# Performance work log

Hardware: AMD Instinct MI355X
Metric: run time of the kernel (lower is better)

## Reference

```python
import jax, jax.numpy as jnp
import numpy as np

S, G, N, E = 4, 3, 20000, 320000   # seq_len, num_graphs, nodes, edges
DIN = HID = OUT = 64


def setup_inputs() -> dict:
    key = jax.random.key(0)
    ks = jax.random.split(key, 12)
    s = 0.1  # weight scale ~ Glorot-ish for d=64
    return {
        "x": jax.random.normal(ks[0], (S, G, N, DIN), jnp.float32),
        "edge_index": jax.random.randint(ks[1], (S, G, 2, E), 0, N, dtype=jnp.int32),
        "W1l": jax.random.normal(ks[2], (G, DIN, HID), jnp.float32) * s,
        "W1r": jax.random.normal(ks[3], (G, DIN, HID), jnp.float32) * s,
        "b1": jnp.zeros((G, HID), jnp.float32),
        "W2l": jax.random.normal(ks[4], (G, HID, OUT), jnp.float32) * s,
        "W2r": jax.random.normal(ks[5], (G, HID, OUT), jnp.float32) * s,
        "b2": jnp.zeros((G, OUT), jnp.float32),
        "Wih": jax.random.normal(ks[6], (4 * OUT, OUT), jnp.float32) * s,
        "Whh": jax.random.normal(ks[7], (4 * OUT, OUT), jnp.float32) * s,
        "bih": jnp.zeros((4 * OUT,), jnp.float32),
        "bhh": jnp.zeros((4 * OUT,), jnp.float32),
    }


def _sage(x, ei, Wl, Wr, b):
    # PyG SAGEConv(aggr='mean'): out = mean_{j->i}(x_j) @ Wl + x_i @ Wr + b
    src, dst = ei[0], ei[1]
    n = x.shape[0]
    msg = jax.ops.segment_sum(x[src], dst, num_segments=n)          # [N, d]
    cnt = jax.ops.segment_sum(jnp.ones((ei.shape[1], 1), x.dtype), dst, num_segments=n)
    mean = jnp.where(cnt > 0, msg / jnp.maximum(cnt, 1.0), 0.0)
    return mean @ Wl + x @ Wr + b


def _gnn(x, ei, Wl1, Wr1, bb1, Wl2, Wr2, bb2):
    h = jnp.tanh(_sage(x, ei, Wl1, Wr1, bb1))
    return jnp.tanh(_sage(h, ei, Wl2, Wr2, bb2))


def reference(x, edge_index, W1l, W1r, b1, W2l, W2r, b2, Wih, Whh, bih, bhh):
    # vmap over graphs (each graph has its own conv weights), then over timesteps
    per_graph = jax.vmap(_gnn, in_axes=(0, 0, 0, 0, 0, 0, 0, 0))
    per_seq = jax.vmap(per_graph, in_axes=(0, 0, None, None, None, None, None, None))
    h = per_seq(x, edge_index, W1l, W1r, b1, W2l, W2r, b2)          # [S, G, N, OUT]
    # torch: per timestep stack graphs [G,N,O] -> transpose -> [N,G,O]; cat over seq on dim0
    lstm_in = jnp.transpose(h, (0, 2, 1, 3)).reshape(S * N, G, OUT)  # [B, T=G, OUT]
    B = lstm_in.shape[0]

    def step(carry, xt):
        hp, cp = carry
        gates = xt @ Wih.T + hp @ Whh.T + bih + bhh                 # [B, 4*OUT]
        i, f, g, o = jnp.split(gates, 4, axis=-1)                   # torch gate order i,f,g,o
        c = jax.nn.sigmoid(f) * cp + jax.nn.sigmoid(i) * jnp.tanh(g)
        hn = jax.nn.sigmoid(o) * jnp.tanh(c)
        return (hn, c), None

    init = (jnp.zeros((B, OUT), x.dtype), jnp.zeros((B, OUT), x.dtype))
    (h_last, _), _ = jax.lax.scan(step, init, jnp.transpose(lstm_in, (1, 0, 2)))
    return h_last  # [S*N, OUT] == lstm_out[:, -1, :].squeeze()
```

## Files before the change

kernel.cpp:

```cpp
#include <hip/hip_runtime.h>
#include <math.h>

#define S 4
#define G 3
#define NN 20000
#define EE 320000
#define D 64
#define SG (S*G)

#define RGS 32
#define RNODES2 625
#define BCAP 12000
#define CHUNKA 100

#define LTILES 314
#define LTASKS (12*LTILES)
#define LPERX  (LTASKS/8)

static __device__ __forceinline__ float rcpf(float x){ return __builtin_amdgcn_rcpf(x); }
static __device__ __forceinline__ float sigmf(float x){ return rcpf(1.0f + __expf(-x)); }
static __device__ __forceinline__ float tanhf_fast(float x){
    float t = __expf(2.0f*x);
    return 1.0f - 2.0f*rcpf(t + 1.0f);
}

static __device__ __forceinline__ unsigned short f2bf(float f){
    union { float f; unsigned u; } v; v.f = f;
    unsigned r = v.u + 0x7FFF + ((v.u >> 16) & 1);
    return (unsigned short)(r >> 16);
}

typedef short bf16x8 __attribute__((ext_vector_type(8)));
typedef float f32x4  __attribute__((ext_vector_type(4)));


__global__ __launch_bounds__(256) void binA_kernel(const int* __restrict__ ei,
                                                   int* __restrict__ bcur,
                                                   int* __restrict__ bkt){
    __shared__ int wcnt[4*RGS];
    __shared__ int wb[4*RGS];
    int chunk = blockIdx.x, sg = blockIdx.y;
    int tid = threadIdx.x, w = tid >> 6;
    const int* srcp = ei + (size_t)(sg*2 + 0)*EE;
    const int* dstp = ei + (size_t)(sg*2 + 1)*EE;
    const int EPC = EE/CHUNKA;
    int start = chunk*EPC, end = start + EPC;

    for (int it = 0; it < (EPC + 1023)/1024; ++it){
        if (tid < 4*RGS) wcnt[tid] = 0;
        __syncthreads();
        int e = start + it*1024 + tid*4;
        bool valid = e < end;
        int d_[4], s_[4], r_[4], dl_[4], rk_[4];
        if (valid){
            int4 d4 = *(const int4*)&dstp[e];
            int4 s4 = *(const int4*)&srcp[e];
            d_[0]=d4.x; d_[1]=d4.y; d_[2]=d4.z; d_[3]=d4.w;
            s_[0]=s4.x; s_[1]=s4.y; s_[2]=s4.z; s_[3]=s4.w;
            #pragma unroll
            for (int j = 0; j < 4; ++j){
                int r = d_[j] / RNODES2;
                r_[j]  = r;
                dl_[j] = d_[j] - r*RNODES2;
                rk_[j] = atomicAdd(&wcnt[w*RGS + r], 1);
            }
        }
        __syncthreads();
        if (tid < RGS){
            int c0 = wcnt[0*RGS+tid], c1 = wcnt[1*RGS+tid];
            int c2 = wcnt[2*RGS+tid], c3 = wcnt[3*RGS+tid];
            int tot = c0+c1+c2+c3;
            int gb = 0;
            if (tot > 0) gb = atomicAdd(&bcur[sg*RGS + tid], tot);
            wb[0*RGS+tid] = gb;
            wb[1*RGS+tid] = gb + c0;
            wb[2*RGS+tid] = gb + c0 + c1;
            wb[3*RGS+tid] = gb + c0 + c1 + c2;
        }
        __syncthreads();
        if (valid){
            #pragma unroll
            for (int j = 0; j < 4; ++j){
                int pos = wb[w*RGS + r_[j]] + rk_[j];
                if (pos < BCAP)
                    bkt[(size_t)(sg*RGS + r_[j])*BCAP + pos] = (dl_[j] << 15) | s_[j];
            }
        }
    }
}


__global__ __launch_bounds__(256) void buildB_kernel(int* __restrict__ bkt,
                                                     const int* __restrict__ bcur,
                                                     int* __restrict__ off2,
                                                     int* __restrict__ deg2){
    __shared__ int hist[RNODES2];
    __shared__ int pref[RNODES2];
    __shared__ int seg[BCAP];
    __shared__ int sums[256];
    int sg = blockIdx.x / RGS, rg = blockIdx.x % RGS;
    int tid = threadIdx.x;
    int cnt = bcur[sg*RGS + rg];
    if (cnt > BCAP) cnt = BCAP;
    size_t base = (size_t)(sg*RGS + rg)*BCAP;

    for (int i = tid; i < RNODES2; i += 256) hist[i] = 0;
    __syncthreads();
    for (int j = tid; j < cnt; j += 256)
        atomicAdd(&hist[bkt[base + j] >> 15], 1);
    __syncthreads();

    int lo = tid*3, hi = min(lo+3, RNODES2);
    int s = 0;
    for (int i = lo; i < hi; ++i) s += hist[i];
    sums[tid] = s; __syncthreads();
    for (int ofs = 1; ofs < 256; ofs <<= 1){
        int v = (tid >= ofs) ? sums[tid-ofs] : 0;
        __syncthreads();
        sums[tid] += v;
        __syncthreads();
    }
    int run = sums[tid] - s;
    int gnode = sg*NN + rg*RNODES2;
    for (int i = lo; i < hi; ++i){
        pref[i] = run;
        off2[gnode + i] = (int)base + run;
        deg2[gnode + i] = hist[i];
        run += hist[i];
    }
    __syncthreads();

    for (int j = tid; j < cnt; j += 256){
        int p = bkt[base + j];
        int slot = atomicAdd(&pref[p >> 15], 1);
        seg[slot] = p & 0x7FFF;
    }
    __syncthreads();

    for (int j = tid; j < cnt; j += 256) bkt[base + j] = seg[j];
}


__global__ __launch_bounds__(256) void convert_kernel(const float* __restrict__ x,
                                                      unsigned short* __restrict__ xb){
    int idx = blockIdx.x*256 + threadIdx.x;
    if (idx >= SG*NN*16) return;
    float4 v = ((const float4*)x)[idx];
    uint2 pk;
    pk.x = (unsigned)f2bf(v.x) | ((unsigned)f2bf(v.y) << 16);
    pk.y = (unsigned)f2bf(v.z) | ((unsigned)f2bf(v.w) << 16);
    ((uint2*)xb)[idx] = pk;
}


__global__ __launch_bounds__(256) void wprep2_kernel(const float* __restrict__ W1l,
                                                     const float* __restrict__ W1r,
                                                     const float* __restrict__ W2l,
                                                     const float* __restrict__ W2r,
                                                     const float* __restrict__ Wih,
                                                     const float* __restrict__ Whh,
                                                     const float* __restrict__ bih,
                                                     const float* __restrict__ bhh,
                                                     unsigned short* __restrict__ WL1,
                                                     unsigned short* __restrict__ WL2,
                                                     unsigned short* __restrict__ Wt,
                                                     float* __restrict__ bc){
    int idx = blockIdx.x*256 + threadIdx.x;
    if (idx < 24576){
        int g = idx >> 13, rem = idx & 8191, col = rem >> 7, k = rem & 127;
        float v = (k < 64) ? W1l[((size_t)g*64 + k)*64 + col]
                           : W1r[((size_t)g*64 + (k-64))*64 + col];
        WL1[idx] = f2bf(v);
    } else if (idx < 49152){
        int t = idx - 24576;
        int g = t >> 13, rem = t & 8191, col = rem >> 7, k = rem & 127;
        float v = (k < 64) ? W2l[((size_t)g*64 + k)*64 + col]
                           : W2r[((size_t)g*64 + (k-64))*64 + col];
        WL2[t] = f2bf(v);
    } else if (idx < 81920){
        int t = idx - 49152;
        int col = t >> 7, k = t & 127;
        float v = (k < 64) ? Wih[col*64 + k] : Whh[col*64 + (k - 64)];
        Wt[t] = f2bf(v);
    } else if (idx < 82176){
        int t = idx - 81920;
        bc[t] = bih[t] + bhh[t];
    }
}


#define WP 72

__global__ __launch_bounds__(256) void layer_kernel(const unsigned short* __restrict__ xb,
                                                    const int* __restrict__ off2,
                                                    const int* __restrict__ deg2,
                                                    const int* __restrict__ csr,
                                                    const unsigned short* __restrict__ WL,
                                                    const float* __restrict__ bias,
                                                    unsigned short* __restrict__ outb){
    __shared__ unsigned short sM[4][16*WP];
    __shared__ unsigned short sO[4][16*WP];
    int L = blockIdx.x;
    int xcd = L & 7, k = L >> 3;
    int task = xcd*LPERX + k;
    int sg = task / LTILES;
    int tile = task - sg*LTILES;
    if (tile >= (NN + 63)/64) return;
    int g = sg % G;
    int tid = threadIdx.x;
    int row0 = tile*64;
    const unsigned short* inb = xb + (size_t)sg*NN*D;

    int wave = tid >> 6, lane = tid & 63;
    int i0 = row0 + wave*16;

    {
        int gp = lane >> 3, fl = lane & 7;
        int ii = min(i0 + (lane & 15), NN-1);
        int val = (lane < 16) ? off2[sg*NN + ii] : ((lane < 32) ? deg2[sg*NN + ii] : 0);
        int r0loc = gp, r1loc = 8 + gp;
        int a0  = __shfl(val, r0loc, 64);
        int dg0 = __shfl(val, 16 + r0loc, 64);
        int a1  = __shfl(val, r1loc, 64);
        int dg1 = __shfl(val, 16 + r1loc, 64);
        if (i0 + r0loc >= NN) dg0 = 0;
        if (i0 + r1loc >= NN) dg1 = 0;
        float acc0[8] = {0,0,0,0,0,0,0,0};
        float acc1[8] = {0,0,0,0,0,0,0,0};
        int mx = max(dg0, dg1);
        for (int base = 0; base < mx; base += 8){
            int my0 = 0, my1 = 0;
            if (base + fl < dg0) my0 = csr[a0 + base + fl];
            if (base + fl < dg1) my1 = csr[a1 + base + fl];
            uint4 v0[8], v1[8];
            #pragma unroll
            for (int j = 0; j < 8; ++j){
                int n0j = __shfl(my0, gp*8 + j, 64);
                int n1j = __shfl(my1, gp*8 + j, 64);
                v0[j] = (uint4){0,0,0,0};
                v1[j] = (uint4){0,0,0,0};
                if (base + j < dg0) v0[j] = *(const uint4*)&inb[(size_t)n0j*D + fl*8];
                if (base + j < dg1) v1[j] = *(const uint4*)&inb[(size_t)n1j*D + fl*8];
            }
            #pragma unroll
            for (int j = 0; j < 8; ++j){
                acc0[0] += __uint_as_float(v0[j].x << 16);
                acc0[1] += __uint_as_float(v0[j].x & 0xFFFF0000u);
                acc0[2] += __uint_as_float(v0[j].y << 16);
                acc0[3] += __uint_as_float(v0[j].y & 0xFFFF0000u);
                acc0[4] += __uint_as_float(v0[j].z << 16);
                acc0[5] += __uint_as_float(v0[j].z & 0xFFFF0000u);
                acc0[6] += __uint_as_float(v0[j].w << 16);
                acc0[7] += __uint_as_float(v0[j].w & 0xFFFF0000u);
                acc1[0] += __uint_as_float(v1[j].x << 16);
                acc1[1] += __uint_as_float(v1[j].x & 0xFFFF0000u);
                acc1[2] += __uint_as_float(v1[j].y << 16);
                acc1[3] += __uint_as_float(v1[j].y & 0xFFFF0000u);
                acc1[4] += __uint_as_float(v1[j].z << 16);
                acc1[5] += __uint_as_float(v1[j].z & 0xFFFF0000u);
                acc1[6] += __uint_as_float(v1[j].w << 16);
                acc1[7] += __uint_as_float(v1[j].w & 0xFFFF0000u);
            }
        }
        float inv0 = (dg0 > 0) ? rcpf((float)dg0) : 0.0f;
        float inv1 = (dg1 > 0) ? rcpf((float)dg1) : 0.0f;
        uint4 pk;
        pk.x = (unsigned)f2bf(acc0[0]*inv0) | ((unsigned)f2bf(acc0[1]*inv0) << 16);
        pk.y = (unsigned)f2bf(acc0[2]*inv0) | ((unsigned)f2bf(acc0[3]*inv0) << 16);
        pk.z = (unsigned)f2bf(acc0[4]*inv0) | ((unsigned)f2bf(acc0[5]*inv0) << 16);
        pk.w = (unsigned)f2bf(acc0[6]*inv0) | ((unsigned)f2bf(acc0[7]*inv0) << 16);
        *(uint4*)&sM[wave][r0loc*WP + fl*8] = pk;
        pk.x = (unsigned)f2bf(acc1[0]*inv1) | ((unsigned)f2bf(acc1[1]*inv1) << 16);
        pk.y = (unsigned)f2bf(acc1[2]*inv1) | ((unsigned)f2bf(acc1[3]*inv1) << 16);
        pk.z = (unsigned)f2bf(acc1[4]*inv1) | ((unsigned)f2bf(acc1[5]*inv1) << 16);
        pk.w = (unsigned)f2bf(acc1[6]*inv1) | ((unsigned)f2bf(acc1[7]*inv1) << 16);
        *(uint4*)&sM[wave][r1loc*WP + fl*8] = pk;
    }

    int n0 = lane & 15, q = lane >> 4;
    const unsigned short* WLg = WL + (size_t)g*64*128;
    f32x4 accv[4];
    #pragma unroll
    for (int ct = 0; ct < 4; ++ct) accv[ct] = (f32x4){0.f,0.f,0.f,0.f};
    int irow = min(i0 + n0, NN-1);
    #pragma unroll
    for (int kc = 0; kc < 4; ++kc){
        bf16x8 af;
        if (kc < 2) af = *(const bf16x8*)&sM[wave][n0*WP + kc*32 + q*8];
        else        af = *(const bf16x8*)&inb[(size_t)irow*D + (kc-2)*32 + q*8];
        #pragma unroll
        for (int ct = 0; ct < 4; ++ct){
            bf16x8 bfr = *(const bf16x8*)&WLg[(ct*16 + n0)*128 + kc*32 + q*8];
            accv[ct] = __builtin_amdgcn_mfma_f32_16x16x32_bf16(af, bfr, accv[ct], 0, 0, 0);
        }
    }
    #pragma unroll
    for (int ct = 0; ct < 4; ++ct){
        float bv = bias[g*64 + ct*16 + n0];
        #pragma unroll
        for (int reg = 0; reg < 4; ++reg)
            sO[wave][(q*4+reg)*WP + ct*16 + n0] = f2bf(tanhf_fast(accv[ct][reg] + bv));
    }
    #pragma unroll
    for (int pass = 0; pass < 2; ++pass){
        int rloc = pass*8 + (lane >> 3), chunk = lane & 7;
        int i = i0 + rloc;
        if (i < NN){
            uint4 v = *(const uint4*)&sO[wave][rloc*WP + chunk*8];
            *(uint4*)&outb[((size_t)sg*NN + i)*D + chunk*8] = v;
        }
    }
}


__global__ __launch_bounds__(256) void lstm_kernel(const unsigned short* __restrict__ h2b,
                                                   const unsigned short* __restrict__ Wt,
                                                   const float* __restrict__ bc,
                                                   float* __restrict__ out){
    __shared__ unsigned short sH[64*WP];
    int tid = threadIdx.x;
    int b0 = blockIdx.x * 64;
    int wave = tid >> 6, lane = tid & 63;
    int n0 = lane & 15, q = lane >> 4;
    int jcol = wave*16 + n0;

    float bb[4];
    #pragma unroll
    for (int T = 0; T < 4; ++T) bb[T] = bc[T*64 + jcol];

    float c[4][4];
    #pragma unroll
    for (int rt = 0; rt < 4; ++rt)
        #pragma unroll
        for (int reg = 0; reg < 4; ++reg) c[rt][reg] = 0.0f;

    int s_[4], n_[4];
    #pragma unroll
    for (int rt = 0; rt < 4; ++rt){
        int b = b0 + rt*16 + n0;
        s_[rt] = b / NN; n_[rt] = b - s_[rt]*NN;
    }

    #pragma unroll
    for (int t = 0; t < G; ++t){
        f32x4 accv[4][4];
        #pragma unroll
        for (int rt = 0; rt < 4; ++rt)
            #pragma unroll
            for (int T = 0; T < 4; ++T) accv[rt][T] = (f32x4){0.f,0.f,0.f,0.f};

        int nkc = (t == 0) ? 2 : 4;
        #pragma unroll
        for (int kc = 0; kc < 4; ++kc){
            if (kc >= nkc) break;
            bf16x8 af[4];
            #pragma unroll
            for (int rt = 0; rt < 4; ++rt){
                if (kc < 2) af[rt] = *(const bf16x8*)&h2b[((size_t)(s_[rt]*G + t)*NN + n_[rt])*D + kc*32 + q*8];
                else        af[rt] = *(const bf16x8*)&sH[(rt*16 + n0)*WP + (kc-2)*32 + q*8];
            }
            #pragma unroll
            for (int T = 0; T < 4; ++T){
                int ct = T*4 + wave;
                bf16x8 bfr = *(const bf16x8*)&Wt[(ct*16 + n0)*128 + kc*32 + q*8];
                #pragma unroll
                for (int rt = 0; rt < 4; ++rt)
                    accv[rt][T] = __builtin_amdgcn_mfma_f32_16x16x32_bf16(af[rt], bfr, accv[rt][T], 0, 0, 0);
            }
        }
        if (t > 0) __syncthreads();

        #pragma unroll
        for (int rt = 0; rt < 4; ++rt){
            #pragma unroll
            for (int reg = 0; reg < 4; ++reg){
                float ig = sigmf(accv[rt][0][reg] + bb[0]);
                float fg = sigmf(accv[rt][1][reg] + bb[1]);
                float gg = tanhf_fast(accv[rt][2][reg] + bb[2]);
                float og = sigmf(accv[rt][3][reg] + bb[3]);
                float cn = fg*c[rt][reg] + ig*gg;
                c[rt][reg] = cn;
                float hv = og * tanhf_fast(cn);
                int row = rt*16 + q*4 + reg;
                if (t < G-1) sH[row*WP + jcol] = f2bf(hv);
                else         out[(size_t)(b0 + row)*D + jcol] = hv;
            }
        }
        if (t < G-1) __syncthreads();
    }
}


extern "C" void kernel_launch(void* const* d_in, const int* in_sizes, int n_in,
                              void* d_out, int out_size, void* d_ws, size_t ws_size,
                              hipStream_t stream) {
    const float* x   = (const float*)d_in[0];
    const int*   ei  = (const int*)  d_in[1];
    const float* W1l = (const float*)d_in[2];
    const float* W1r = (const float*)d_in[3];
    const float* b1  = (const float*)d_in[4];
    const float* W2l = (const float*)d_in[5];
    const float* W2r = (const float*)d_in[6];
    const float* b2  = (const float*)d_in[7];
    const float* Wih = (const float*)d_in[8];
    const float* Whh = (const float*)d_in[9];
    const float* bih = (const float*)d_in[10];
    const float* bhh = (const float*)d_in[11];
    float* out = (float*)d_out;

    char* ws = (char*)d_ws;
    size_t cur = 0;
    auto alloc = [&](size_t bytes)->void*{
        cur = (cur + 255) & ~(size_t)255;
        void* p = ws + cur; cur += bytes; return p;
    };
    int*   bkt  = (int*)alloc((size_t)SG*RGS*BCAP*4);
    int*   bcur = (int*)alloc((size_t)SG*RGS*4);
    int*   off2 = (int*)alloc((size_t)SG*NN*4);
    int*   deg2 = (int*)alloc((size_t)SG*NN*4);
    unsigned short* xb  = (unsigned short*)alloc((size_t)SG*NN*D*2);
    unsigned short* h1b = (unsigned short*)alloc((size_t)SG*NN*D*2);
    unsigned short* h2b = (unsigned short*)alloc((size_t)SG*NN*D*2);
    unsigned short* WL1 = (unsigned short*)alloc((size_t)G*64*128*2);
    unsigned short* WL2 = (unsigned short*)alloc((size_t)G*64*128*2);
    unsigned short* Wt  = (unsigned short*)alloc((size_t)256*128*2);
    float* bc   = (float*)alloc((size_t)256*4);
    (void)ws_size; (void)in_sizes; (void)n_in; (void)out_size;

    (void)hipMemsetAsync(bcur, 0, (size_t)SG*RGS*4, stream);

    convert_kernel<<<(SG*NN*16 + 255)/256, 256, 0, stream>>>(x, xb);
    binA_kernel  <<<dim3(CHUNKA, SG), 256, 0, stream>>>(ei, bcur, bkt);
    buildB_kernel<<<SG*RGS, 256, 0, stream>>>(bkt, bcur, off2, deg2);
    wprep2_kernel<<<321, 256, 0, stream>>>(W1l, W1r, W2l, W2r, Wih, Whh, bih, bhh,
                                           WL1, WL2, Wt, bc);

    layer_kernel<<<LTASKS, 256, 0, stream>>>(xb,  off2, deg2, bkt, WL1, b1, h1b);
    layer_kernel<<<LTASKS, 256, 0, stream>>>(h1b, off2, deg2, bkt, WL2, b2, h2b);

    lstm_kernel <<<(S*NN)/64, 256, 0, stream>>>(h2b, Wt, bc, out);
}
```

Before: 373.8 us.

## Aggregate neighbors via MFMA with padded CSR segments and zero-row sentinel

```diff
diff --git a/kernel.cpp b/kernel.cpp
--- a/kernel.cpp
+++ b/kernel.cpp
@@ -10,7 +10,7 @@
 
 #define RGS 32
 #define RNODES2 625
-#define BCAP 12000
+#define BCAP 14336
 #define CHUNKA 100
 
 #define LTILES 314
@@ -112,7 +112,7 @@
 
     int lo = tid*3, hi = min(lo+3, RNODES2);
     int s = 0;
-    for (int i = lo; i < hi; ++i) s += hist[i];
+    for (int i = lo; i < hi; ++i) s += (hist[i] + 3) & ~3;
     sums[tid] = s; __syncthreads();
     for (int ofs = 1; ofs < 256; ofs <<= 1){
         int v = (tid >= ofs) ? sums[tid-ofs] : 0;
@@ -126,18 +126,19 @@
         pref[i] = run;
         off2[gnode + i] = (int)base + run;
         deg2[gnode + i] = hist[i];
-        run += hist[i];
+        run += (hist[i] + 3) & ~3;
     }
     __syncthreads();
 
     for (int j = tid; j < cnt; j += 256){
         int p = bkt[base + j];
         int slot = atomicAdd(&pref[p >> 15], 1);
-        seg[slot] = p & 0x7FFF;
+        if (slot < BCAP) seg[slot] = p & 0x7FFF;
     }
     __syncthreads();
 
-    for (int j = tid; j < cnt; j += 256) bkt[base + j] = seg[j];
+    int padtot = min(sums[255], BCAP);
+    for (int j = tid; j < padtot; j += 256) bkt[base + j] = seg[j];
 }
 
 
@@ -191,14 +192,13 @@
 
 #define WP 72
 
-__global__ __launch_bounds__(256) void layer_kernel(const unsigned short* __restrict__ xb,
+__global__ __launch_bounds__(256,3) void layer_kernel(const unsigned short* __restrict__ xb,
                                                     const int* __restrict__ off2,
                                                     const int* __restrict__ deg2,
                                                     const int* __restrict__ csr,
                                                     const unsigned short* __restrict__ WL,
                                                     const float* __restrict__ bias,
                                                     unsigned short* __restrict__ outb){
-    __shared__ unsigned short sM[4][16*WP];
     __shared__ unsigned short sO[4][16*WP];
     int L = blockIdx.x;
     int xcd = L & 7, k = L >> 3;
@@ -210,104 +210,117 @@
     int tid = threadIdx.x;
     int row0 = tile*64;
     const unsigned short* inb = xb + (size_t)sg*NN*D;
+    const char* inbc = (const char*)inb;
 
     int wave = tid >> 6, lane = tid & 63;
     int i0 = row0 + wave*16;
-
-    {
-        int gp = lane >> 3, fl = lane & 7;
-        int ii = min(i0 + (lane & 15), NN-1);
-        int val = (lane < 16) ? off2[sg*NN + ii] : ((lane < 32) ? deg2[sg*NN + ii] : 0);
-        int r0loc = gp, r1loc = 8 + gp;
-        int a0  = __shfl(val, r0loc, 64);
-        int dg0 = __shfl(val, 16 + r0loc, 64);
-        int a1  = __shfl(val, r1loc, 64);
-        int dg1 = __shfl(val, 16 + r1loc, 64);
-        if (i0 + r0loc >= NN) dg0 = 0;
-        if (i0 + r1loc >= NN) dg1 = 0;
-        float acc0[8] = {0,0,0,0,0,0,0,0};
-        float acc1[8] = {0,0,0,0,0,0,0,0};
-        int mx = max(dg0, dg1);
-        for (int base = 0; base < mx; base += 8){
-            int my0 = 0, my1 = 0;
-            if (base + fl < dg0) my0 = csr[a0 + base + fl];
-            if (base + fl < dg1) my1 = csr[a1 + base + fl];
-            uint4 v0[8], v1[8];
-            #pragma unroll
-            for (int j = 0; j < 8; ++j){
-                int n0j = __shfl(my0, gp*8 + j, 64);
-                int n1j = __shfl(my1, gp*8 + j, 64);
-                v0[j] = (uint4){0,0,0,0};
-                v1[j] = (uint4){0,0,0,0};
-                if (base + j < dg0) v0[j] = *(const uint4*)&inb[(size_t)n0j*D + fl*8];
-                if (base + j < dg1) v1[j] = *(const uint4*)&inb[(size_t)n1j*D + fl*8];
-            }
-            #pragma unroll
-            for (int j = 0; j < 8; ++j){
-                acc0[0] += __uint_as_float(v0[j].x << 16);
-                acc0[1] += __uint_as_float(v0[j].x & 0xFFFF0000u);
-                acc0[2] += __uint_as_float(v0[j].y << 16);
-                acc0[3] += __uint_as_float(v0[j].y & 0xFFFF0000u);
-                acc0[4] += __uint_as_float(v0[j].z << 16);
-                acc0[5] += __uint_as_float(v0[j].z & 0xFFFF0000u);
-                acc0[6] += __uint_as_float(v0[j].w << 16);
-                acc0[7] += __uint_as_float(v0[j].w & 0xFFFF0000u);
-                acc1[0] += __uint_as_float(v1[j].x << 16);
-                acc1[1] += __uint_as_float(v1[j].x & 0xFFFF0000u);
-                acc1[2] += __uint_as_float(v1[j].y << 16);
-                acc1[3] += __uint_as_float(v1[j].y & 0xFFFF0000u);
-                acc1[4] += __uint_as_float(v1[j].z << 16);
-                acc1[5] += __uint_as_float(v1[j].z & 0xFFFF0000u);
-                acc1[6] += __uint_as_float(v1[j].w << 16);
-                acc1[7] += __uint_as_float(v1[j].w & 0xFFFF0000u);
-            }
-        }
-        float inv0 = (dg0 > 0) ? rcpf((float)dg0) : 0.0f;
-        float inv1 = (dg1 > 0) ? rcpf((float)dg1) : 0.0f;
-        uint4 pk;
-        pk.x = (unsigned)f2bf(acc0[0]*inv0) | ((unsigned)f2bf(acc0[1]*inv0) << 16);
-        pk.y = (unsigned)f2bf(acc0[2]*inv0) | ((unsigned)f2bf(acc0[3]*inv0) << 16);
-        pk.z = (unsigned)f2bf(acc0[4]*inv0) | ((unsigned)f2bf(acc0[5]*inv0) << 16);
-        pk.w = (unsigned)f2bf(acc0[6]*inv0) | ((unsigned)f2bf(acc0[7]*inv0) << 16);
-        *(uint4*)&sM[wave][r0loc*WP + fl*8] = pk;
-        pk.x = (unsigned)f2bf(acc1[0]*inv1) | ((unsigned)f2bf(acc1[1]*inv1) << 16);
-        pk.y = (unsigned)f2bf(acc1[2]*inv1) | ((unsigned)f2bf(acc1[3]*inv1) << 16);
-        pk.z = (unsigned)f2bf(acc1[4]*inv1) | ((unsigned)f2bf(acc1[5]*inv1) << 16);
-        pk.w = (unsigned)f2bf(acc1[6]*inv1) | ((unsigned)f2bf(acc1[7]*inv1) << 16);
-        *(uint4*)&sM[wave][r1loc*WP + fl*8] = pk;
-    }
-
-    int n0 = lane & 15, q = lane >> 4;
+    int r = lane & 15, q = lane >> 4;
+    unsigned qb = (unsigned)(q << 4);
+
     const unsigned short* WLg = WL + (size_t)g*64*128;
-    f32x4 accv[4];
-    #pragma unroll
-    for (int ct = 0; ct < 4; ++ct) accv[ct] = (f32x4){0.f,0.f,0.f,0.f};
-    int irow = min(i0 + n0, NN-1);
-    #pragma unroll
-    for (int kc = 0; kc < 4; ++kc){
-        bf16x8 af;
-        if (kc < 2) af = *(const bf16x8*)&sM[wave][n0*WP + kc*32 + q*8];
-        else        af = *(const bf16x8*)&inb[(size_t)irow*D + (kc-2)*32 + q*8];
-        #pragma unroll
-        for (int ct = 0; ct < 4; ++ct){
-            bf16x8 bfr = *(const bf16x8*)&WLg[(ct*16 + n0)*128 + kc*32 + q*8];
-            accv[ct] = __builtin_amdgcn_mfma_f32_16x16x32_bf16(af, bfr, accv[ct], 0, 0, 0);
-        }
-    }
+    bf16x8 B0[4], B1[4];
     #pragma unroll
     for (int ct = 0; ct < 4; ++ct){
-        float bv = bias[g*64 + ct*16 + n0];
+        B0[ct] = *(const bf16x8*)&WLg[(ct*16 + r)*128 + 0*32 + q*8];
+        B1[ct] = *(const bf16x8*)&WLg[(ct*16 + r)*128 + 1*32 + q*8];
+    }
+
+    int i = i0 + r;
+    int dg = 0, a = 0;
+    if (i < NN){ a = off2[sg*NN + i]; dg = deg2[sg*NN + i]; }
+    int mx = dg;
+    mx = max(mx, __shfl_xor(mx, 1));
+    mx = max(mx, __shfl_xor(mx, 2));
+    mx = max(mx, __shfl_xor(mx, 4));
+    mx = max(mx, __shfl_xor(mx, 8));
+
+    int irow = min(i, NN-1);
+    bf16x8 S0 = *(const bf16x8*)(inbc + (((unsigned)irow) << 7) + qb);
+    bf16x8 S1 = *(const bf16x8*)(inbc + (((unsigned)irow) << 7) + qb + 64);
+
+    unsigned zoff = (((unsigned)((SG - sg)*NN)) << 7) + qb;
+
+    f32x4 acc[4];
+    #pragma unroll
+    for (int ct = 0; ct < 4; ++ct) acc[ct] = (f32x4){0.f,0.f,0.f,0.f};
+
+    if (mx > 0){
+        int4 ix = *(const int4*)&csr[a];
+        bf16x8 A0[4], A1[4];
+        {
+            int ii[4] = {ix.x, ix.y, ix.z, ix.w};
+            #pragma unroll
+            for (int j = 0; j < 4; ++j){
+                unsigned off = (((unsigned)ii[j]) << 7) + qb;
+                if (j >= dg) off = zoff;
+                A0[j] = *(const bf16x8*)(inbc + off);
+                A1[j] = *(const bf16x8*)(inbc + off + 64);
+            }
+        }
+        int4 ixn = *(const int4*)&csr[a + 4];
+        for (int s4 = 0; s4 < mx; s4 += 4){
+            bf16x8 N0[4], N1[4];
+            {
+                int ii[4] = {ixn.x, ixn.y, ixn.z, ixn.w};
+                #pragma unroll
+                for (int j = 0; j < 4; ++j){
+                    unsigned off = (((unsigned)ii[j]) << 7) + qb;
+                    if (s4 + 4 + j >= dg) off = zoff;
+                    N0[j] = *(const bf16x8*)(inbc + off);
+                    N1[j] = *(const bf16x8*)(inbc + off + 64);
+                }
+            }
+            ixn = *(const int4*)&csr[a + s4 + 8];
+            __builtin_amdgcn_s_setprio(1);
+            #pragma unroll
+            for (int j = 0; j < 4; ++j){
+                #pragma unroll
+                for (int ct = 0; ct < 4; ++ct)
+                    acc[ct] = __builtin_amdgcn_mfma_f32_16x16x32_bf16(A0[j], B0[ct], acc[ct], 0, 0, 0);
+                #pragma unroll
+                for (int ct = 0; ct < 4; ++ct)
+                    acc[ct] = __builtin_amdgcn_mfma_f32_16x16x32_bf16(A1[j], B1[ct], acc[ct], 0, 0, 0);
+            }
+            __builtin_amdgcn_s_setprio(0);
+            #pragma unroll
+            for (int j = 0; j < 4; ++j){ A0[j] = N0[j]; A1[j] = N1[j]; }
+        }
+    }
+
+    float inv[4];
+    #pragma unroll
+    for (int reg = 0; reg < 4; ++reg){
+        int d = __shfl(dg, (q << 2) | reg, 16);
+        inv[reg] = (d > 0) ? rcpf((float)d) : 0.0f;
+    }
+    #pragma unroll
+    for (int ct = 0; ct < 4; ++ct)
         #pragma unroll
         for (int reg = 0; reg < 4; ++reg)
-            sO[wave][(q*4+reg)*WP + ct*16 + n0] = f2bf(tanhf_fast(accv[ct][reg] + bv));
+            acc[ct][reg] *= inv[reg];
+
+    #pragma unroll
+    for (int ct = 0; ct < 4; ++ct){
+        bf16x8 b2 = *(const bf16x8*)&WLg[(ct*16 + r)*128 + 2*32 + q*8];
+        acc[ct] = __builtin_amdgcn_mfma_f32_16x16x32_bf16(S0, b2, acc[ct], 0, 0, 0);
+        bf16x8 b3 = *(const bf16x8*)&WLg[(ct*16 + r)*128 + 3*32 + q*8];
+        acc[ct] = __builtin_amdgcn_mfma_f32_16x16x32_bf16(S1, b3, acc[ct], 0, 0, 0);
+    }
+
+    #pragma unroll
+    for (int ct = 0; ct < 4; ++ct){
+        float bv = bias[g*64 + ct*16 + r];
+        #pragma unroll
+        for (int reg = 0; reg < 4; ++reg)
+            sO[wave][(q*4+reg)*WP + ct*16 + r] = f2bf(tanhf_fast(acc[ct][reg] + bv));
     }
     #pragma unroll
     for (int pass = 0; pass < 2; ++pass){
         int rloc = pass*8 + (lane >> 3), chunk = lane & 7;
-        int i = i0 + rloc;
-        if (i < NN){
+        int i2 = i0 + rloc;
+        if (i2 < NN){
             uint4 v = *(const uint4*)&sO[wave][rloc*WP + chunk*8];
-            *(uint4*)&outb[((size_t)sg*NN + i)*D + chunk*8] = v;
+            *(uint4*)&outb[((size_t)sg*NN + i2)*D + chunk*8] = v;
         }
     }
 }
@@ -418,8 +431,8 @@
     int*   bcur = (int*)alloc((size_t)SG*RGS*4);
     int*   off2 = (int*)alloc((size_t)SG*NN*4);
     int*   deg2 = (int*)alloc((size_t)SG*NN*4);
-    unsigned short* xb  = (unsigned short*)alloc((size_t)SG*NN*D*2);
-    unsigned short* h1b = (unsigned short*)alloc((size_t)SG*NN*D*2);
+    unsigned short* xb  = (unsigned short*)alloc(((size_t)SG*NN + 1)*D*2);
+    unsigned short* h1b = (unsigned short*)alloc(((size_t)SG*NN + 1)*D*2);
     unsigned short* h2b = (unsigned short*)alloc((size_t)SG*NN*D*2);
     unsigned short* WL1 = (unsigned short*)alloc((size_t)G*64*128*2);
     unsigned short* WL2 = (unsigned short*)alloc((size_t)G*64*128*2);
@@ -428,6 +441,8 @@
     (void)ws_size; (void)in_sizes; (void)n_in; (void)out_size;
 
     (void)hipMemsetAsync(bcur, 0, (size_t)SG*RGS*4, stream);
+    (void)hipMemsetAsync(xb  + (size_t)SG*NN*D, 0, (size_t)D*2, stream);
+    (void)hipMemsetAsync(h1b + (size_t)SG*NN*D, 0, (size_t)D*2, stream);
 
     convert_kernel<<<(SG*NN*16 + 255)/256, 256, 0, stream>>>(x, xb);
     binA_kernel  <<<dim3(CHUNKA, SG), 256, 0, stream>>>(ei, bcur, bkt);
```

New measurement: 462.2 us. +23.7%, slower.
